# Performance work log

Measured on AMD Instinct MI355X. Metric: run time of the kernel, lower is better.

Reference implementation:

```python
import jax, jax.numpy as jnp
import numpy as np

B, S, D, H = 4, 2048, 1024, 4096
EPS = 1e-5

def _layernorm(x, g, b):
    mu = jnp.mean(x, axis=-1, keepdims=True)
    var = jnp.mean(jnp.square(x - mu), axis=-1, keepdims=True)
    return (x - mu) * jax.lax.rsqrt(var + EPS) * g + b

def setup_inputs() -> dict:
    key = jax.random.key(0)
    ks = jax.random.split(key, 8)
    s = lambda d: 1.0 / np.sqrt(d)
    return {
        "x": jax.random.normal(ks[0], (B, S, D), jnp.float32),
        "Wq": jax.random.normal(ks[1], (D, D), jnp.float32) * s(D),
        "bq": jnp.zeros((D,), jnp.float32),
        "Wk": jax.random.normal(ks[2], (D, D), jnp.float32) * s(D),
        "bk": jnp.zeros((D,), jnp.float32),
        "Wv": jax.random.normal(ks[3], (D, D), jnp.float32) * s(D),
        "bv": jnp.zeros((D,), jnp.float32),
        "Wo": jax.random.normal(ks[4], (D, D), jnp.float32) * s(D),
        "bo": jnp.zeros((D,), jnp.float32),
        "g1": jnp.ones((D,), jnp.float32),
        "be1": jnp.zeros((D,), jnp.float32),
        "g2": jnp.ones((D,), jnp.float32),
        "be2": jnp.zeros((D,), jnp.float32),
        "W1": jax.random.normal(ks[5], (D, H), jnp.float32) * s(D),
        "b1": jnp.zeros((H,), jnp.float32),
        "W2": jax.random.normal(ks[6], (H, D), jnp.float32) * s(H),
        "b2": jnp.zeros((D,), jnp.float32),
    }

def reference(x, Wq, bq, Wk, bk, Wv, bv, Wo, bo, g1, be1, g2, be2, W1, b1, W2, b2):
    # pre-norm self-attention + residual
    xn = _layernorm(x, g1, be1)
    q = xn @ Wq + bq            # [B,S,D]
    k = xn @ Wk + bk
    v = xn @ Wv + bv
    scale = 1.0 / jnp.sqrt(jnp.float32(D))
    scores = jnp.einsum("bsd,btd->bst", q, k) * scale  # [B,S,S]
    attn = jax.nn.softmax(scores, axis=-1)
    attn_out = jnp.einsum("bst,btd->bsd", attn, v) @ Wo + bo
    x = x + attn_out
    # pre-norm MLP + residual
    xn2 = _layernorm(x, g2, be2)
    ffn = jax.nn.relu(xn2 @ W1 + b1) @ W2 + b2
    out = x + ffn
    return out, attn
```

## Files before the change

kernel.cpp:

```cpp
#include <hip/hip_runtime.h>
#include <hip/hip_bf16.h>


typedef __bf16 bf16_t;
typedef __bf16 bf16x8 __attribute__((ext_vector_type(8)));
typedef float  f32x4  __attribute__((ext_vector_type(4)));

#define EPI_QKV            0
#define EPI_F32_SCALE      2
#define EPI_BF16           3
#define EPI_F32_BIAS_RES   4
#define EPI_BF16_RELU_BIAS 5

__device__ __forceinline__ void gl_lds16(const bf16_t* g, void* l) {
  __builtin_amdgcn_global_load_lds(
      (const __attribute__((address_space(1))) void*)g,
      (__attribute__((address_space(3))) void*)l, 16, 0, 0);
}

template<int BM, int EPI>
__global__ __launch_bounds__(512, 2)
void gemm8p(const bf16_t* __restrict__ A, const bf16_t* __restrict__ B,
            float* __restrict__ Cf, bf16_t* __restrict__ Cb,
            bf16_t* __restrict__ Cb2, bf16_t* __restrict__ Cb3,
            const float* __restrict__ bias, const float* __restrict__ bias2,
            const float* __restrict__ bias3, const float* __restrict__ resid,
            int M, int N, int K, long sAb, long sBb, long sCb, float scale)
{
  constexpr int BN  = 256;
  constexpr int WTM = BM / 2;
  constexpr int MF  = WTM / 16;
  constexpr int NF  = 4;
  constexpr int LA  = BM / 128;
  constexpr int LB  = 2;
  constexpr int L   = LA + LB;
  constexpr int L0  = 2;
  constexpr int SBUF = (BM + BN) * 64;
  constexpr int W   = 2 * L;
  __shared__ __align__(16) char lds[4 * SBUF];

  const int tid  = threadIdx.x;
  const int l    = tid & 63;
  const int w    = tid >> 6;
  const int wm   = w >> 2;
  const int wn   = w & 3;

  const int nx = gridDim.x, ny = gridDim.y;
  const int tot = nx * ny * gridDim.z;
  int id = blockIdx.x + nx * (blockIdx.y + ny * blockIdx.z);
  const int cpx = tot >> 3;
  int s = (id & 7) * cpx + (id >> 3);
  const int bx = s % nx; int rq = s / nx;
  const int by = rq % ny; const int bz = rq / ny;

  const bf16_t* Ab = A + (long)bz * sAb;
  const bf16_t* Bb = B + (long)bz * sBb;
  const int m0 = by * BM, n0 = bx * BN;
  const int NT = K >> 5;

  const int srow = w * 16 + (l >> 2);
  const int scol = ((l & 3) ^ ((l >> 3) & 3)) * 8;
  const bf16_t* srcA[LA]; const bf16_t* srcB[LB];
#pragma unroll
  for (int q = 0; q < LA; ++q) srcA[q] = Ab + (long)(m0 + q * 128 + srow) * K + scol;
#pragma unroll
  for (int q = 0; q < LB; ++q) srcB[q] = Bb + (long)(n0 + q * 128 + srow) * K + scol;
  const int ldsA = w * 1024;
  const int ldsB = BM * 64 + w * 1024;

  const int rA0 = wm * WTM + (l & 15);
  const int rB0 = wn * 64 + (l & 15);
  const int xoff = 16 * ((l >> 4) ^ ((l >> 1) & 3));

  f32x4 acc[MF][NF] = {};
  bf16x8 afr[MF / 2], bfr[NF];

#pragma unroll
  for (int d = 0; d < 3; ++d) {
    char* bufS = lds + d * SBUF;
    const long kst = (long)d * 32;
#pragma unroll
    for (int q = 0; q < LA; ++q) gl_lds16(srcA[q] + kst, bufS + ldsA + q * 8192);
#pragma unroll
    for (int q = 0; q < LB; ++q) gl_lds16(srcB[q] + kst, bufS + ldsB + q * 8192);
  }
  asm volatile("s_waitcnt vmcnt(%0)" :: "n"(W) : "memory");
  __builtin_amdgcn_s_barrier();
  __builtin_amdgcn_sched_barrier(0);

  for (int t = 0; t < NT; ++t) {
    const char* bufR = lds + (t & 3) * SBUF;
    char* bufS = lds + ((t + 3) & 3) * SBUF;
    const int tst = t + 3;
    const long kst = (long)((tst < NT) ? tst : (NT - 1)) * 32;

#pragma unroll
    for (int nf = 0; nf < NF; ++nf)
      bfr[nf] = *(const bf16x8*)(bufR + BM * 64 + (rB0 + nf * 16) * 64 + xoff);
#pragma unroll
    for (int mf = 0; mf < MF / 2; ++mf)
      afr[mf] = *(const bf16x8*)(bufR + (rA0 + mf * 16) * 64 + xoff);
#pragma unroll
    for (int q = 0; q < L0; ++q) {
      if (q < LA) gl_lds16(srcA[q] + kst, bufS + ldsA + q * 8192);
      else        gl_lds16(srcB[q - LA] + kst, bufS + ldsB + (q - LA) * 8192);
    }
    __builtin_amdgcn_s_barrier();
    __builtin_amdgcn_s_setprio(1);
#pragma unroll
    for (int mf = 0; mf < MF / 2; ++mf)
#pragma unroll
      for (int nf = 0; nf < NF; ++nf)
        acc[mf][nf] = __builtin_amdgcn_mfma_f32_16x16x32_bf16(afr[mf], bfr[nf], acc[mf][nf], 0, 0, 0);
    __builtin_amdgcn_s_setprio(0);
    __builtin_amdgcn_s_barrier();

#pragma unroll
    for (int mf = 0; mf < MF / 2; ++mf)
      afr[mf] = *(const bf16x8*)(bufR + (rA0 + (MF / 2 + mf) * 16) * 64 + xoff);
#pragma unroll
    for (int q = L0; q < L; ++q) {
      if (q < LA) gl_lds16(srcA[q] + kst, bufS + ldsA + q * 8192);
      else        gl_lds16(srcB[q - LA] + kst, bufS + ldsB + (q - LA) * 8192);
    }
    __builtin_amdgcn_s_barrier();
    __builtin_amdgcn_s_setprio(1);
#pragma unroll
    for (int mf = 0; mf < MF / 2; ++mf)
#pragma unroll
      for (int nf = 0; nf < NF; ++nf)
        acc[MF / 2 + mf][nf] = __builtin_amdgcn_mfma_f32_16x16x32_bf16(afr[mf], bfr[nf], acc[MF / 2 + mf][nf], 0, 0, 0);
    __builtin_amdgcn_s_setprio(0);
    asm volatile("s_waitcnt vmcnt(%0)" :: "n"(W) : "memory");
    __builtin_amdgcn_s_barrier();
    __builtin_amdgcn_sched_barrier(0);
  }

  asm volatile("s_waitcnt vmcnt(0)" ::: "memory");

  const int colB0 = n0 + wn * 64 + (l & 15);
  const int rowB0 = m0 + wm * WTM + ((l >> 4) << 2);
#pragma unroll
  for (int mi = 0; mi < MF; ++mi) {
#pragma unroll
    for (int ni = 0; ni < NF; ++ni) {
      const int col = colB0 + ni * 16;
#pragma unroll
      for (int j = 0; j < 4; ++j) {
        const int row = rowB0 + mi * 16 + j;
        const float v = acc[mi][ni][j];
        if constexpr (EPI == EPI_F32_SCALE) {
          Cf[sCb * bz + (long)row * N + col] = v * scale;
        } else if constexpr (EPI == EPI_QKV) {
          if (col < 1024)      Cb [(long)row * 1024 + col]        = (bf16_t)(v + bias[col]);
          else if (col < 2048) Cb2[(long)row * 1024 + col - 1024] = (bf16_t)(v + bias2[col - 1024]);
          else {
            const int c2 = col - 2048, b = row >> 11, tt = row & 2047;
            Cb3[((long)b * 1024 + c2) * 2048 + tt] = (bf16_t)(v + bias3[c2]);
          }
        } else if constexpr (EPI == EPI_BF16) {
          Cb[sCb * bz + (long)row * N + col] = (bf16_t)v;
        } else if constexpr (EPI == EPI_F32_BIAS_RES) {
          Cf[(long)row * N + col] = v + bias[col] + resid[(long)row * N + col];
        } else {
          const float u = v + bias[col];
          Cb[(long)row * N + col] = (bf16_t)(u > 0.f ? u : 0.f);
        }
      }
    }
  }
}

__global__ __launch_bounds__(256)
void ln_kernel(const float* __restrict__ x, const float* __restrict__ g,
               const float* __restrict__ be, bf16_t* __restrict__ out)
{
  const long row = blockIdx.x;
  const float4 v = *(const float4*)(x + row * 1024 + threadIdx.x * 4);
  float s  = v.x + v.y + v.z + v.w;
  float s2 = v.x * v.x + v.y * v.y + v.z * v.z + v.w * v.w;
  __shared__ float red[10];
  const int lane = threadIdx.x & 63, w = threadIdx.x >> 6;
#pragma unroll
  for (int off = 32; off; off >>= 1) {
    s  += __shfl_down(s, off);
    s2 += __shfl_down(s2, off);
  }
  if (lane == 0) { red[w] = s; red[4 + w] = s2; }
  __syncthreads();
  if (threadIdx.x == 0) {
    const float ts = red[0] + red[1] + red[2] + red[3];
    const float t2 = red[4] + red[5] + red[6] + red[7];
    const float mu = ts * (1.f / 1024.f);
    const float var = t2 * (1.f / 1024.f) - mu * mu;
    red[8] = mu;
    red[9] = rsqrtf(var + 1e-5f);
  }
  __syncthreads();
  const float mu = red[8], rinv = red[9];
  const int c = threadIdx.x * 4;
  const float4 gv = *(const float4*)(g + c);
  const float4 bv = *(const float4*)(be + c);
  bf16_t* o = out + row * 1024 + c;
  o[0] = (bf16_t)((v.x - mu) * rinv * gv.x + bv.x);
  o[1] = (bf16_t)((v.y - mu) * rinv * gv.y + bv.y);
  o[2] = (bf16_t)((v.z - mu) * rinv * gv.z + bv.z);
  o[3] = (bf16_t)((v.w - mu) * rinv * gv.w + bv.w);
}

__global__ __launch_bounds__(256)
void softmax_kernel(float* __restrict__ sc, bf16_t* __restrict__ ab)
{
  const long row = blockIdx.x;
  float* sr = sc + row * 2048;
  const int t0 = threadIdx.x * 8;
  const float4 a = *(const float4*)(sr + t0);
  const float4 b = *(const float4*)(sr + t0 + 4);
  float mx = fmaxf(fmaxf(fmaxf(a.x, a.y), fmaxf(a.z, a.w)),
                   fmaxf(fmaxf(b.x, b.y), fmaxf(b.z, b.w)));
  __shared__ float red[4];
  __shared__ float bc[2];
  const int lane = threadIdx.x & 63, w = threadIdx.x >> 6;
#pragma unroll
  for (int off = 32; off; off >>= 1) mx = fmaxf(mx, __shfl_down(mx, off));
  if (lane == 0) red[w] = mx;
  __syncthreads();
  if (threadIdx.x == 0) bc[0] = fmaxf(fmaxf(red[0], red[1]), fmaxf(red[2], red[3]));
  __syncthreads();
  const float m = bc[0];
  float e[8];
  e[0] = __expf(a.x - m); e[1] = __expf(a.y - m); e[2] = __expf(a.z - m); e[3] = __expf(a.w - m);
  e[4] = __expf(b.x - m); e[5] = __expf(b.y - m); e[6] = __expf(b.z - m); e[7] = __expf(b.w - m);
  float s = e[0] + e[1] + e[2] + e[3] + e[4] + e[5] + e[6] + e[7];
#pragma unroll
  for (int off = 32; off; off >>= 1) s += __shfl_down(s, off);
  __syncthreads();
  if (lane == 0) red[w] = s;
  __syncthreads();
  if (threadIdx.x == 0) bc[1] = 1.f / (red[0] + red[1] + red[2] + red[3]);
  __syncthreads();
  const float inv = bc[1];
  float4 oa, ob;
  oa.x = e[0] * inv; oa.y = e[1] * inv; oa.z = e[2] * inv; oa.w = e[3] * inv;
  ob.x = e[4] * inv; ob.y = e[5] * inv; ob.z = e[6] * inv; ob.w = e[7] * inv;
  *(float4*)(sr + t0)     = oa;
  *(float4*)(sr + t0 + 4) = ob;
  bf16x8 o8;
  o8[0] = (bf16_t)oa.x; o8[1] = (bf16_t)oa.y; o8[2] = (bf16_t)oa.z; o8[3] = (bf16_t)oa.w;
  o8[4] = (bf16_t)ob.x; o8[5] = (bf16_t)ob.y; o8[6] = (bf16_t)ob.z; o8[7] = (bf16_t)ob.w;
  *(bf16x8*)(ab + row * 2048 + t0) = o8;
}

__global__ __launch_bounds__(256)
void transpose_cvt(const float* __restrict__ W, bf16_t* __restrict__ WT, int R, int C)
{
  __shared__ float t[32][33];
  const int c0 = blockIdx.x * 32, r0 = blockIdx.y * 32;
  const int tx = threadIdx.x & 31, ty = threadIdx.x >> 5;
#pragma unroll
  for (int i = 0; i < 32; i += 8)
    t[ty + i][tx] = W[(long)(r0 + ty + i) * C + c0 + tx];
  __syncthreads();
#pragma unroll
  for (int i = 0; i < 32; i += 8)
    WT[(long)(c0 + ty + i) * R + r0 + tx] = (bf16_t)t[tx][ty + i];
}

extern "C" void kernel_launch(void* const* d_in, const int* in_sizes, int n_in,
                              void* d_out, int out_size, void* d_ws, size_t ws_size,
                              hipStream_t stream)
{
  const float* x   = (const float*)d_in[0];
  const float* Wq  = (const float*)d_in[1];
  const float* bq  = (const float*)d_in[2];
  const float* Wk  = (const float*)d_in[3];
  const float* bk  = (const float*)d_in[4];
  const float* Wv  = (const float*)d_in[5];
  const float* bv  = (const float*)d_in[6];
  const float* Wo  = (const float*)d_in[7];
  const float* bo  = (const float*)d_in[8];
  const float* g1  = (const float*)d_in[9];
  const float* be1 = (const float*)d_in[10];
  const float* g2  = (const float*)d_in[11];
  const float* be2 = (const float*)d_in[12];
  const float* W1  = (const float*)d_in[13];
  const float* b1  = (const float*)d_in[14];
  const float* W2  = (const float*)d_in[15];
  const float* b2  = (const float*)d_in[16];

  float* out   = (float*)d_out;
  float* attnF = out + 8192L * 1024;

  char* ws = (char*)d_ws;
  const size_t MB = 1024 * 1024;
  bf16_t* WqkvT = (bf16_t*)(ws + 0 * MB);
  bf16_t* WoT   = (bf16_t*)(ws + 6 * MB);
  bf16_t* W1T   = (bf16_t*)(ws + 8 * MB);
  bf16_t* W2T   = (bf16_t*)(ws + 16 * MB);
  bf16_t* xn    = (bf16_t*)(ws + 24 * MB);
  bf16_t* qB    = (bf16_t*)(ws + 40 * MB);
  bf16_t* kB    = (bf16_t*)(ws + 56 * MB);
  bf16_t* vT    = (bf16_t*)(ws + 72 * MB);
  bf16_t* atB   = (bf16_t*)(ws + 88 * MB);
  float*  x2    = (float* )(ws + 120 * MB);
  bf16_t* hB    = (bf16_t*)(ws + 56 * MB);

  transpose_cvt<<<dim3(32, 32),  256, 0, stream>>>(Wq, WqkvT,                 1024, 1024);
  transpose_cvt<<<dim3(32, 32),  256, 0, stream>>>(Wk, WqkvT + 1024L * 1024,  1024, 1024);
  transpose_cvt<<<dim3(32, 32),  256, 0, stream>>>(Wv, WqkvT + 2048L * 1024,  1024, 1024);
  transpose_cvt<<<dim3(32, 32),  256, 0, stream>>>(Wo, WoT, 1024, 1024);
  transpose_cvt<<<dim3(128, 32), 256, 0, stream>>>(W1, W1T, 1024, 4096);
  transpose_cvt<<<dim3(32, 128), 256, 0, stream>>>(W2, W2T, 4096, 1024);

  ln_kernel<<<8192, 256, 0, stream>>>(x, g1, be1, xn);

  gemm8p<128, EPI_QKV><<<dim3(12, 64, 1), 512, 0, stream>>>(
      xn, WqkvT, nullptr, qB, kB, vT, bq, bk, bv, nullptr,
      8192, 3072, 1024, 0, 0, 0, 1.f);

  gemm8p<256, EPI_F32_SCALE><<<dim3(8, 8, 4), 512, 0, stream>>>(
      qB, kB, attnF, nullptr, nullptr, nullptr, nullptr, nullptr, nullptr, nullptr,
      2048, 2048, 1024, 2048L * 1024, 2048L * 1024, 2048L * 2048, 0.03125f);

  softmax_kernel<<<8192, 256, 0, stream>>>(attnF, atB);

  gemm8p<128, EPI_BF16><<<dim3(4, 16, 4), 512, 0, stream>>>(
      atB, vT, nullptr, qB, nullptr, nullptr, nullptr, nullptr, nullptr, nullptr,
      2048, 1024, 2048, 2048L * 2048, 1024L * 2048, 2048L * 1024, 1.f);

  gemm8p<128, EPI_F32_BIAS_RES><<<dim3(4, 64, 1), 512, 0, stream>>>(
      qB, WoT, x2, nullptr, nullptr, nullptr, bo, nullptr, nullptr, x,
      8192, 1024, 1024, 0, 0, 0, 1.f);

  ln_kernel<<<8192, 256, 0, stream>>>(x2, g2, be2, xn);

  gemm8p<256, EPI_BF16_RELU_BIAS><<<dim3(16, 32, 1), 512, 0, stream>>>(
      xn, W1T, nullptr, hB, nullptr, nullptr, b1, nullptr, nullptr, nullptr,
      8192, 4096, 1024, 0, 0, 0, 1.f);
  gemm8p<128, EPI_F32_BIAS_RES><<<dim3(4, 64, 1), 512, 0, stream>>>(
      hB, W2T, out, nullptr, nullptr, nullptr, b2, nullptr, nullptr, x2,
      8192, 1024, 4096, 0, 0, 0, 1.f);
}
```

Before: 458.9 us.

## Add BK=64 triple-buffered 128x256 GEMM and separate V transpose kernel

Adds a new gemm128 kernel for the BM=128 GEMMs: QKV, attn@V, Wo and W2. It uses a K-tile of 64 with triple-buffered LDS (3x48KB), runs one block per CU, and does two MFMA sub-steps per tile to halve the barrier and loop overhead per K element. The QKV epilogue now writes V row-major into scratch space borrowed from the attention output buffer. A new transpose_bf kernel then produces vT, replacing the strided scattered stores of the old epilogue. This trades occupancy (1 block/CU, large LDS) and an extra transpose pass for better memory coalescing and deeper prefetch.

Result: faster. 422.5 us (-7.9%).

```diff
diff --git a/kernel.cpp b/kernel.cpp
--- a/kernel.cpp
+++ b/kernel.cpp
@@ -22,9 +22,7 @@
 __global__ __launch_bounds__(512, 2)
 void gemm8p(const bf16_t* __restrict__ A, const bf16_t* __restrict__ B,
             float* __restrict__ Cf, bf16_t* __restrict__ Cb,
-            bf16_t* __restrict__ Cb2, bf16_t* __restrict__ Cb3,
-            const float* __restrict__ bias, const float* __restrict__ bias2,
-            const float* __restrict__ bias3, const float* __restrict__ resid,
+            const float* __restrict__ bias, const float* __restrict__ resid,
             int M, int N, int K, long sAb, long sBb, long sCb, float scale)
 {
   constexpr int BN  = 256;
@@ -39,11 +37,11 @@
   constexpr int W   = 2 * L;
   __shared__ __align__(16) char lds[4 * SBUF];
 
-  const int tid  = threadIdx.x;
-  const int l    = tid & 63;
-  const int w    = tid >> 6;
-  const int wm   = w >> 2;
-  const int wn   = w & 3;
+  const int tid = threadIdx.x;
+  const int l   = tid & 63;
+  const int w   = tid >> 6;
+  const int wm  = w >> 2;
+  const int wn  = w & 3;
 
   const int nx = gridDim.x, ny = gridDim.y;
   const int tot = nx * ny * gridDim.z;
@@ -135,7 +133,6 @@
     __builtin_amdgcn_s_barrier();
     __builtin_amdgcn_sched_barrier(0);
   }
-
   asm volatile("s_waitcnt vmcnt(0)" ::: "memory");
 
   const int colB0 = n0 + wn * 64 + (l & 15);
@@ -151,23 +148,167 @@
         const float v = acc[mi][ni][j];
         if constexpr (EPI == EPI_F32_SCALE) {
           Cf[sCb * bz + (long)row * N + col] = v * scale;
-        } else if constexpr (EPI == EPI_QKV) {
-          if (col < 1024)      Cb [(long)row * 1024 + col]        = (bf16_t)(v + bias[col]);
-          else if (col < 2048) Cb2[(long)row * 1024 + col - 1024] = (bf16_t)(v + bias2[col - 1024]);
-          else {
-            const int c2 = col - 2048, b = row >> 11, tt = row & 2047;
-            Cb3[((long)b * 1024 + c2) * 2048 + tt] = (bf16_t)(v + bias3[c2]);
-          }
-        } else if constexpr (EPI == EPI_BF16) {
-          Cb[sCb * bz + (long)row * N + col] = (bf16_t)v;
-        } else if constexpr (EPI == EPI_F32_BIAS_RES) {
-          Cf[(long)row * N + col] = v + bias[col] + resid[(long)row * N + col];
         } else {
           const float u = v + bias[col];
           Cb[(long)row * N + col] = (bf16_t)(u > 0.f ? u : 0.f);
         }
       }
     }
+  }
+}
+
+template<int EPI>
+__global__ __launch_bounds__(512, 1)
+void gemm128(const bf16_t* __restrict__ A, const bf16_t* __restrict__ B,
+             float* __restrict__ Cf, bf16_t* __restrict__ Cb,
+             bf16_t* __restrict__ Cb2, bf16_t* __restrict__ Cb3,
+             const float* __restrict__ bias, const float* __restrict__ bias2,
+             const float* __restrict__ bias3, const float* __restrict__ resid,
+             int M, int N, int K, long sAb, long sBb, long sCb)
+{
+  constexpr int SBUF = 49152;
+  __shared__ __align__(16) char lds[3 * SBUF];
+  const int tid = threadIdx.x;
+  const int l   = tid & 63;
+  const int w   = tid >> 6;
+  const int wm  = w >> 2, wn = w & 3;
+
+  const int nx = gridDim.x, ny = gridDim.y;
+  const int tot = nx * ny * gridDim.z;
+  int id = blockIdx.x + nx * (blockIdx.y + ny * blockIdx.z);
+  const int cpx = tot >> 3;
+  int sid = (id & 7) * cpx + (id >> 3);
+  const int bx = sid % nx; int rq = sid / nx;
+  const int by = rq % ny; const int bz = rq / ny;
+
+  const bf16_t* Ab = A + (long)bz * sAb;
+  const bf16_t* Bb = B + (long)bz * sBb;
+  const int m0 = by * 128, n0 = bx * 256;
+  const int NT = K >> 6;
+
+  const int scol = ((l & 7) ^ (l >> 3)) * 8;
+  const bf16_t* srcA = Ab + (long)(m0 + 16 * w + (l >> 3)) * K + scol;
+  const bf16_t* srcB = Bb + (long)(n0 + 32 * w + (l >> 3)) * K + scol;
+  const int dA = w * 2048 + l * 16;
+  const int dB = 16384 + w * 4096 + l * 16;
+
+  const int rA = wm * 64 + (l & 15);
+  const int rB = wn * 64 + (l & 15);
+  const int xo = ((l >> 4) ^ (l & 7)) * 16;
+  const int aoff = rA * 128 + xo;
+  const int boff = 16384 + rB * 128 + xo;
+
+  f32x4 acc[4][4] = {};
+  bf16x8 af[4], bv[4];
+
+  {
+    char* b0 = lds; char* b1 = lds + SBUF;
+#pragma unroll
+    for (int q = 0; q < 2; ++q) gl_lds16(srcA + (long)q * 8 * K, b0 + dA + q * 1024);
+#pragma unroll
+    for (int q = 0; q < 4; ++q) gl_lds16(srcB + (long)q * 8 * K, b0 + dB + q * 1024);
+#pragma unroll
+    for (int q = 0; q < 2; ++q) gl_lds16(srcA + (long)q * 8 * K + 64, b1 + dA + q * 1024);
+#pragma unroll
+    for (int q = 0; q < 4; ++q) gl_lds16(srcB + (long)q * 8 * K + 64, b1 + dB + q * 1024);
+  }
+  asm volatile("s_waitcnt vmcnt(6)" ::: "memory");
+  __builtin_amdgcn_s_barrier();
+  __builtin_amdgcn_sched_barrier(0);
+
+  int ir = 0, is = 2;
+  for (int t = 0; t < NT; ++t) {
+    const char* bufR = lds + ir * SBUF;
+    char* bufS = lds + is * SBUF;
+    const int tst = (t + 2 < NT) ? t + 2 : NT - 1;
+    const long kst = (long)tst * 64;
+
+#pragma unroll
+    for (int nf = 0; nf < 4; ++nf) bv[nf] = *(const bf16x8*)(bufR + boff + nf * 2048);
+#pragma unroll
+    for (int mf = 0; mf < 4; ++mf) af[mf] = *(const bf16x8*)(bufR + aoff + mf * 2048);
+    gl_lds16(srcA + kst,                 bufS + dA);
+    gl_lds16(srcA + (long)8 * K + kst,   bufS + dA + 1024);
+    gl_lds16(srcB + kst,                 bufS + dB);
+    __builtin_amdgcn_s_barrier();
+    __builtin_amdgcn_s_setprio(1);
+#pragma unroll
+    for (int mf = 0; mf < 4; ++mf)
+#pragma unroll
+      for (int nf = 0; nf < 4; ++nf)
+        acc[mf][nf] = __builtin_amdgcn_mfma_f32_16x16x32_bf16(af[mf], bv[nf], acc[mf][nf], 0, 0, 0);
+    __builtin_amdgcn_s_setprio(0);
+    __builtin_amdgcn_s_barrier();
+
+#pragma unroll
+    for (int nf = 0; nf < 4; ++nf) bv[nf] = *(const bf16x8*)(bufR + ((boff + nf * 2048) ^ 64));
+#pragma unroll
+    for (int mf = 0; mf < 4; ++mf) af[mf] = *(const bf16x8*)(bufR + ((aoff + mf * 2048) ^ 64));
+    gl_lds16(srcB + (long)8 * K + kst,   bufS + dB + 1024);
+    gl_lds16(srcB + (long)16 * K + kst,  bufS + dB + 2048);
+    gl_lds16(srcB + (long)24 * K + kst,  bufS + dB + 3072);
+    __builtin_amdgcn_s_barrier();
+    __builtin_amdgcn_s_setprio(1);
+#pragma unroll
+    for (int mf = 0; mf < 4; ++mf)
+#pragma unroll
+      for (int nf = 0; nf < 4; ++nf)
+        acc[mf][nf] = __builtin_amdgcn_mfma_f32_16x16x32_bf16(af[mf], bv[nf], acc[mf][nf], 0, 0, 0);
+    __builtin_amdgcn_s_setprio(0);
+    asm volatile("s_waitcnt vmcnt(6)" ::: "memory");
+    __builtin_amdgcn_s_barrier();
+    __builtin_amdgcn_sched_barrier(0);
+    ir = (ir == 2) ? 0 : ir + 1;
+    is = (is == 2) ? 0 : is + 1;
+  }
+  asm volatile("s_waitcnt vmcnt(0)" ::: "memory");
+
+  const int colB0 = n0 + wn * 64 + (l & 15);
+  const int rowB0 = m0 + wm * 64 + ((l >> 4) << 2);
+#pragma unroll
+  for (int mi = 0; mi < 4; ++mi) {
+#pragma unroll
+    for (int ni = 0; ni < 4; ++ni) {
+      const int col = colB0 + ni * 16;
+#pragma unroll
+      for (int j = 0; j < 4; ++j) {
+        const int row = rowB0 + mi * 16 + j;
+        const float v = acc[mi][ni][j];
+        if constexpr (EPI == EPI_QKV) {
+          if (col < 1024)      Cb [(long)row * 1024 + col]        = (bf16_t)(v + bias[col]);
+          else if (col < 2048) Cb2[(long)row * 1024 + col - 1024] = (bf16_t)(v + bias2[col - 1024]);
+          else                 Cb3[(long)row * 1024 + col - 2048] = (bf16_t)(v + bias3[col - 2048]);
+        } else if constexpr (EPI == EPI_BF16) {
+          Cb[sCb * bz + (long)row * N + col] = (bf16_t)v;
+        } else {
+          Cf[(long)row * N + col] = v + bias[col] + resid[(long)row * N + col];
+        }
+      }
+    }
+  }
+}
+
+__global__ __launch_bounds__(256)
+void transpose_bf(const bf16_t* __restrict__ V, bf16_t* __restrict__ VT)
+{
+  __shared__ __align__(16) bf16_t t[64][72];
+  const int b = blockIdx.z;
+  const int t0 = blockIdx.y * 64, d0 = blockIdx.x * 64;
+  const int r = threadIdx.x >> 3;
+  const int c = (threadIdx.x & 7) * 8;
+  const bf16_t* src = V + ((long)b * 2048 + t0) * 1024 + d0;
+#pragma unroll
+  for (int h = 0; h < 2; ++h)
+    *(bf16x8*)&t[r + 32 * h][c] = *(const bf16x8*)(src + (long)(r + 32 * h) * 1024 + c);
+  __syncthreads();
+  bf16_t* dst = VT + ((long)b * 1024 + d0) * 2048 + t0;
+#pragma unroll
+  for (int h = 0; h < 2; ++h) {
+    const int d = r + 32 * h;
+    bf16x8 o;
+#pragma unroll
+    for (int j = 0; j < 8; ++j) o[j] = t[c + j][d];
+    *(bf16x8*)(dst + (long)d * 2048 + c) = o;
   }
 }
 
@@ -200,12 +341,12 @@
   const float mu = red[8], rinv = red[9];
   const int c = threadIdx.x * 4;
   const float4 gv = *(const float4*)(g + c);
-  const float4 bv = *(const float4*)(be + c);
+  const float4 bvv = *(const float4*)(be + c);
   bf16_t* o = out + row * 1024 + c;
-  o[0] = (bf16_t)((v.x - mu) * rinv * gv.x + bv.x);
-  o[1] = (bf16_t)((v.y - mu) * rinv * gv.y + bv.y);
-  o[2] = (bf16_t)((v.z - mu) * rinv * gv.z + bv.z);
-  o[3] = (bf16_t)((v.w - mu) * rinv * gv.w + bv.w);
+  o[0] = (bf16_t)((v.x - mu) * rinv * gv.x + bvv.x);
+  o[1] = (bf16_t)((v.y - mu) * rinv * gv.y + bvv.y);
+  o[2] = (bf16_t)((v.z - mu) * rinv * gv.z + bvv.z);
+  o[3] = (bf16_t)((v.w - mu) * rinv * gv.w + bvv.w);
 }
 
 __global__ __launch_bounds__(256)
@@ -290,6 +431,7 @@
 
   float* out   = (float*)d_out;
   float* attnF = out + 8192L * 1024;
+  bf16_t* vB   = (bf16_t*)attnF;
 
   char* ws = (char*)d_ws;
   const size_t MB = 1024 * 1024;
@@ -305,39 +447,41 @@
   float*  x2    = (float* )(ws + 120 * MB);
   bf16_t* hB    = (bf16_t*)(ws + 56 * MB);
 
-  transpose_cvt<<<dim3(32, 32),  256, 0, stream>>>(Wq, WqkvT,                 1024, 1024);
-  transpose_cvt<<<dim3(32, 32),  256, 0, stream>>>(Wk, WqkvT + 1024L * 1024,  1024, 1024);
-  transpose_cvt<<<dim3(32, 32),  256, 0, stream>>>(Wv, WqkvT + 2048L * 1024,  1024, 1024);
+  transpose_cvt<<<dim3(32, 32),  256, 0, stream>>>(Wq, WqkvT,                1024, 1024);
+  transpose_cvt<<<dim3(32, 32),  256, 0, stream>>>(Wk, WqkvT + 1024L * 1024, 1024, 1024);
+  transpose_cvt<<<dim3(32, 32),  256, 0, stream>>>(Wv, WqkvT + 2048L * 1024, 1024, 1024);
   transpose_cvt<<<dim3(32, 32),  256, 0, stream>>>(Wo, WoT, 1024, 1024);
   transpose_cvt<<<dim3(128, 32), 256, 0, stream>>>(W1, W1T, 1024, 4096);
   transpose_cvt<<<dim3(32, 128), 256, 0, stream>>>(W2, W2T, 4096, 1024);
 
   ln_kernel<<<8192, 256, 0, stream>>>(x, g1, be1, xn);
 
-  gemm8p<128, EPI_QKV><<<dim3(12, 64, 1), 512, 0, stream>>>(
-      xn, WqkvT, nullptr, qB, kB, vT, bq, bk, bv, nullptr,
-      8192, 3072, 1024, 0, 0, 0, 1.f);
+  gemm128<EPI_QKV><<<dim3(12, 64, 1), 512, 0, stream>>>(
+      xn, WqkvT, nullptr, qB, kB, vB, bq, bk, bv, nullptr,
+      8192, 3072, 1024, 0, 0, 0);
+
+  transpose_bf<<<dim3(16, 32, 4), 256, 0, stream>>>(vB, vT);
 
   gemm8p<256, EPI_F32_SCALE><<<dim3(8, 8, 4), 512, 0, stream>>>(
-      qB, kB, attnF, nullptr, nullptr, nullptr, nullptr, nullptr, nullptr, nullptr,
+      qB, kB, attnF, nullptr, nullptr, nullptr,
       2048, 2048, 1024, 2048L * 1024, 2048L * 1024, 2048L * 2048, 0.03125f);
 
   softmax_kernel<<<8192, 256, 0, stream>>>(attnF, atB);
 
-  gemm8p<128, EPI_BF16><<<dim3(4, 16, 4), 512, 0, stream>>>(
+  gemm128<EPI_BF16><<<dim3(4, 16, 4), 512, 0, stream>>>(
       atB, vT, nullptr, qB, nullptr, nullptr, nullptr, nullptr, nullptr, nullptr,
-      2048, 1024, 2048, 2048L * 2048, 1024L * 2048, 2048L * 1024, 1.f);
-
-  gemm8p<128, EPI_F32_BIAS_RES><<<dim3(4, 64, 1), 512, 0, stream>>>(
+      2048, 1024, 2048, 2048L * 2048, 1024L * 2048, 2048L * 1024);
+
+  gemm128<EPI_F32_BIAS_RES><<<dim3(4, 64, 1), 512, 0, stream>>>(
       qB, WoT, x2, nullptr, nullptr, nullptr, bo, nullptr, nullptr, x,
-      8192, 1024, 1024, 0, 0, 0, 1.f);
+      8192, 1024, 1024, 0, 0, 0);
 
   ln_kernel<<<8192, 256, 0, stream>>>(x2, g2, be2, xn);
 
   gemm8p<256, EPI_BF16_RELU_BIAS><<<dim3(16, 32, 1), 512, 0, stream>>>(
-      xn, W1T, nullptr, hB, nullptr, nullptr, b1, nullptr, nullptr, nullptr,
+      xn, W1T, nullptr, hB, b1, nullptr,
       8192, 4096, 1024, 0, 0, 0, 1.f);
-  gemm8p<128, EPI_F32_BIAS_RES><<<dim3(4, 64, 1), 512, 0, stream>>>(
+  gemm128<EPI_F32_BIAS_RES><<<dim3(4, 64, 1), 512, 0, stream>>>(
       hB, W2T, out, nullptr, nullptr, nullptr, b2, nullptr, nullptr, x2,
-      8192, 1024, 4096, 0, 0, 0, 1.f);
-}
+      8192, 1024, 4096, 0, 0, 0);
+}
```
